# Kernel optimization log

Measured on AMD Instinct MI355X. Metric: run time of the kernel, lower is better.

## Reference

```python
import jax, jax.numpy as jnp
import numpy as np

# MPO config: input_size = output_size = 4096 = 16**3, num_cores = 3, rank = 16
D_IN = 16    # in_leg_dim
D_OUT = 16   # out_leg_dim
RANK = 16
IN_SIZE = D_IN ** 3
OUT_SIZE = D_OUT ** 3
B = 2048     # flattened batch*seq tokens


def setup_inputs() -> dict:
    key = jax.random.key(0)
    ks = jax.random.split(key, 5)
    bound = 1.0 / np.sqrt(IN_SIZE)
    u = lambda k, shp: jax.random.uniform(k, shp, jnp.float32, -bound, bound)
    return {
        "x": jax.random.normal(ks[0], (B, IN_SIZE), dtype=jnp.float32),
        "first_core": u(ks[1], (D_IN, RANK, D_OUT)),        # (in, rank_right, out)
        "middle_core": u(ks[2], (D_IN, RANK, RANK, D_OUT)),  # (in, rank_left, rank_right, out)
        "last_core": u(ks[3], (D_IN, RANK, D_OUT)),          # (in, rank_left, out)
        "bias": u(ks[4], (OUT_SIZE,)),
    }


def reference(x, first_core, middle_core, last_core, bias):
    # Faithful MPO chain contraction, same edge wiring and order as the
    # tensornetwork-based original (contract input legs left-to-right,
    # threading the bond/rank index through the cores).
    xr = x.reshape(-1, D_IN, D_IN, D_IN)                       # (b, i, j, k)
    # contract input leg i with first core -> legs (b, j, k, r, m)
    t = jnp.einsum('bijk,irm->bjkrm', xr, first_core)
    # contract input leg j and bond r with middle core -> (b, k, m, s, n)
    t = jnp.einsum('bjkrm,jrsn->bkmsn', t, middle_core)
    # contract input leg k and bond s with last core -> (b, m, n, o)
    t = jnp.einsum('bkmsn,kso->bmno', t, last_core)
    return t.reshape(-1, OUT_SIZE) + bias
```

## Files before the change

### kernel.cpp

```cpp
#include <hip/hip_runtime.h>

#define DLEG 16
#define IN_SIZE 4096
#define OUT_SIZE 4096
#define BATCH 2048

#define SX 25.4f
#define SW 1.1545455e6f

typedef __attribute__((ext_vector_type(4))) int i32x4;

__device__ __forceinline__ signed char f2i8(float f, float s) {
  int q = __float2int_rn(f * s);
  q = q > 127 ? 127 : (q < -127 ? -127 : q);
  return (signed char)q;
}

__device__ __forceinline__ void async_copy16(const void* g, void* l) {
  __builtin_amdgcn_global_load_lds(
      (const __attribute__((address_space(1))) void*)g,
      (__attribute__((address_space(3))) void*)l, 16, 0, 0);
}

__global__ __launch_bounds__(256) void k_cvt(const float* __restrict__ x,
                                             signed char* __restrict__ xi) {
  const int idx = blockIdx.x * 256 + threadIdx.x;
  const float4* xp = (const float4*)x + (size_t)idx * 4;
  union { int4 v; signed char c[16]; } u;
#pragma unroll
  for (int q = 0; q < 4; ++q) {
    const float4 f = xp[q];
    u.c[q * 4 + 0] = f2i8(f.x, SX);
    u.c[q * 4 + 1] = f2i8(f.y, SX);
    u.c[q * 4 + 2] = f2i8(f.z, SX);
    u.c[q * 4 + 3] = f2i8(f.w, SX);
  }
  ((int4*)xi)[idx] = u.v;
}

__global__ __launch_bounds__(256) void k_build_wt(
    const float* __restrict__ fc, const float* __restrict__ mc,
    const float* __restrict__ lc, signed char* __restrict__ wt) {
  __shared__ float fc_s[256];
  __shared__ float mc_s[4096];
  __shared__ float a_s[1024];
  const int b = blockIdx.x;
  const int mg = blockIdx.y;
  const int i = b >> 4, j = b & 15;
  const int t = threadIdx.x;

  fc_s[t] = fc[i * 256 + t];
#pragma unroll
  for (int q = 0; q < 16; ++q) mc_s[q * 256 + t] = mc[j * 4096 + q * 256 + t];
  __syncthreads();

  {
    const int n = t >> 4, s = t & 15;
    float accm[4] = {0.f, 0.f, 0.f, 0.f};
#pragma unroll
    for (int r = 0; r < 16; ++r) {
      const float mcv = mc_s[r * 256 + s * 16 + n];
#pragma unroll
      for (int ml = 0; ml < 4; ++ml)
        accm[ml] = fmaf(fc_s[r * 16 + mg * 4 + ml], mcv, accm[ml]);
    }
#pragma unroll
    for (int ml = 0; ml < 4; ++ml) a_s[ml * 256 + n * 16 + s] = accm[ml];
  }
  __syncthreads();

  const int k = t & 15, op = (t >> 4) & 3, sel = t >> 6;
  float lcr[4][16];
#pragma unroll
  for (int oo = 0; oo < 4; ++oo)
#pragma unroll
    for (int s = 0; s < 16; ++s)
      lcr[oo][s] = lc[k * 256 + s * 16 + op * 4 + oo];

#pragma unroll
  for (int ml = 0; ml < 4; ++ml) {
#pragma unroll
    for (int nn = 0; nn < 4; ++nn) {
      const int n = sel * 4 + nn;
      const float4* ap = (const float4*)&a_s[ml * 256 + n * 16];
      float av[16];
      ((float4*)av)[0] = ap[0];
      ((float4*)av)[1] = ap[1];
      ((float4*)av)[2] = ap[2];
      ((float4*)av)[3] = ap[3];
      float accv[4] = {0.f, 0.f, 0.f, 0.f};
#pragma unroll
      for (int s = 0; s < 16; ++s) {
#pragma unroll
        for (int oo = 0; oo < 4; ++oo)
          accv[oo] = fmaf(av[s], lcr[oo][s], accv[oo]);
      }
      const size_t colbase =
          (size_t)((mg * 4 + ml) * 256 + n * 16 + op * 4);
#pragma unroll
      for (int oo = 0; oo < 4; ++oo)
        wt[(colbase + oo) * 4096 + b * 16 + k] = f2i8(accv[oo], SW);
    }
  }
}

__global__ __launch_bounds__(256, 2) void k_gemm(
    const signed char* __restrict__ X,
    const signed char* __restrict__ Wt,
    const float* __restrict__ bias,
    float* __restrict__ out) {
  __shared__ signed char As[2][128 * 128];
  __shared__ signed char Bs[2][128 * 128];

  const int t = threadIdx.x;
  const int l = t & 63, w = t >> 6;
  const int wm = w >> 1, wn = w & 1;
  const int m0 = blockIdx.y * 128, n0 = blockIdx.x * 128;

  const signed char* xg[4];
  const signed char* wg[4];
  int ldsoff[4];
#pragma unroll
  for (int u = 0; u < 4; ++u) {
    const int c = u * 256 + t;
    const int row = c >> 3;
    const int slot = (c & 7) ^ (row & 7);
    xg[u] = X + (size_t)(m0 + row) * 4096 + slot * 16;
    wg[u] = Wt + (size_t)(n0 + row) * 4096 + slot * 16;
    ldsoff[u] = c * 16;
  }

  const int arow = wm * 64 + (l & 15);
  const int brow = wn * 64 + (l & 15);
  const int lk = l >> 4;
  const int lx = l & 7;

  i32x4 acc[4][4];
#pragma unroll
  for (int a = 0; a < 4; ++a)
#pragma unroll
    for (int c = 0; c < 4; ++c) acc[a][c] = (i32x4){0, 0, 0, 0};

#pragma unroll
  for (int u = 0; u < 4; ++u) async_copy16(xg[u], As[0] + ldsoff[u]);
#pragma unroll
  for (int u = 0; u < 4; ++u) async_copy16(wg[u], Bs[0] + ldsoff[u]);

  for (int kt = 0; kt < 4096; kt += 128) {
    const int cur = (kt >> 7) & 1;
    __syncthreads();
    if (kt + 128 < 4096) {
#pragma unroll
      for (int u = 0; u < 4; ++u)
        async_copy16(xg[u] + kt + 128, As[cur ^ 1] + ldsoff[u]);
#pragma unroll
      for (int u = 0; u < 4; ++u)
        async_copy16(wg[u] + kt + 128, Bs[cur ^ 1] + ldsoff[u]);
    }

#pragma unroll
    for (int ks = 0; ks < 2; ++ks) {
      const int slot = ((ks * 4 + lk) ^ lx) * 16;
      i32x4 af[4], bf[4];
#pragma unroll
      for (int mi = 0; mi < 4; ++mi)
        af[mi] = *(const i32x4*)&As[cur][(arow + mi * 16) * 128 + slot];
#pragma unroll
      for (int ni = 0; ni < 4; ++ni)
        bf[ni] = *(const i32x4*)&Bs[cur][(brow + ni * 16) * 128 + slot];
#pragma unroll
      for (int mi = 0; mi < 4; ++mi)
#pragma unroll
        for (int ni = 0; ni < 4; ++ni)
          acc[mi][ni] = __builtin_amdgcn_mfma_i32_16x16x64_i8(
              af[mi], bf[ni], acc[mi][ni], 0, 0, 0);
    }
  }

  const float inv = 1.0f / (SX * SW);
#pragma unroll
  for (int ni = 0; ni < 4; ++ni) {
    const int col = n0 + wn * 64 + ni * 16 + (l & 15);
    const float bv = bias[col];
#pragma unroll
    for (int mi = 0; mi < 4; ++mi) {
      const int row = m0 + wm * 64 + mi * 16 + (l >> 4) * 4;
#pragma unroll
      for (int r = 0; r < 4; ++r)
        out[(size_t)(row + r) * 4096 + col] =
            (float)acc[mi][ni][r] * inv + bv;
    }
  }
}

extern "C" void kernel_launch(void* const* d_in, const int* in_sizes, int n_in,
                              void* d_out, int out_size, void* d_ws,
                              size_t ws_size, hipStream_t stream) {
  const float* x    = (const float*)d_in[0];
  const float* fc   = (const float*)d_in[1];
  const float* mc   = (const float*)d_in[2];
  const float* lc   = (const float*)d_in[3];
  const float* bias = (const float*)d_in[4];
  float* out = (float*)d_out;

  signed char* xi = (signed char*)d_ws;
  signed char* wt = xi + (size_t)BATCH * IN_SIZE;

  k_cvt<<<(BATCH * IN_SIZE / 16) / 256, 256, 0, stream>>>(x, xi);
  k_build_wt<<<dim3(256, 4), 256, 0, stream>>>(fc, mc, lc, wt);
  k_gemm<<<dim3(OUT_SIZE / 128, BATCH / 128), 256, 0, stream>>>(xi, wt, bias, out);
}
```

Before: 152.3 us.

## Merge prep kernels into one launch and halve GEMM K-tile for occupancy

The input quantization and weight-building kernels become one launch, with block index choosing the path, which saves a launch and lets both kinds of work run at the same time. The int8 GEMM K-tile shrinks from 128 to 64, which cuts LDS use to 32KB per block, and launch bounds rise to 4 blocks per CU. The LDS swizzle changes to a 4-slot XOR to match. In exchange there are twice as many K iterations and barriers, with less work between syncs to hide load latency.

New measurement: 159.1 us. 4.4% more time.

```diff
diff --git a/kernel.cpp b/kernel.cpp
--- a/kernel.cpp
+++ b/kernel.cpp
@@ -22,32 +22,35 @@
       (__attribute__((address_space(3))) void*)l, 16, 0, 0);
 }
 
-__global__ __launch_bounds__(256) void k_cvt(const float* __restrict__ x,
-                                             signed char* __restrict__ xi) {
-  const int idx = blockIdx.x * 256 + threadIdx.x;
-  const float4* xp = (const float4*)x + (size_t)idx * 4;
-  union { int4 v; signed char c[16]; } u;
-#pragma unroll
-  for (int q = 0; q < 4; ++q) {
-    const float4 f = xp[q];
-    u.c[q * 4 + 0] = f2i8(f.x, SX);
-    u.c[q * 4 + 1] = f2i8(f.y, SX);
-    u.c[q * 4 + 2] = f2i8(f.z, SX);
-    u.c[q * 4 + 3] = f2i8(f.w, SX);
-  }
-  ((int4*)xi)[idx] = u.v;
-}
-
-__global__ __launch_bounds__(256) void k_build_wt(
-    const float* __restrict__ fc, const float* __restrict__ mc,
-    const float* __restrict__ lc, signed char* __restrict__ wt) {
+__global__ __launch_bounds__(256) void k_prep(
+    const float* __restrict__ x, const float* __restrict__ fc,
+    const float* __restrict__ mc, const float* __restrict__ lc,
+    signed char* __restrict__ xi, signed char* __restrict__ wt) {
   __shared__ float fc_s[256];
   __shared__ float mc_s[4096];
   __shared__ float a_s[1024];
-  const int b = blockIdx.x;
-  const int mg = blockIdx.y;
+  const int t = threadIdx.x;
+
+  if (blockIdx.x < 2048) {
+    const int idx = blockIdx.x * 256 + t;
+    const float4* xp = (const float4*)x + (size_t)idx * 4;
+    union { int4 v; signed char c[16]; } u;
+#pragma unroll
+    for (int q = 0; q < 4; ++q) {
+      const float4 f = xp[q];
+      u.c[q * 4 + 0] = f2i8(f.x, SX);
+      u.c[q * 4 + 1] = f2i8(f.y, SX);
+      u.c[q * 4 + 2] = f2i8(f.z, SX);
+      u.c[q * 4 + 3] = f2i8(f.w, SX);
+    }
+    ((int4*)xi)[idx] = u.v;
+    return;
+  }
+
+  const int idx = blockIdx.x - 2048;
+  const int b = idx & 255;
+  const int mg = idx >> 8;
   const int i = b >> 4, j = b & 15;
-  const int t = threadIdx.x;
 
   fc_s[t] = fc[i * 256 + t];
 #pragma unroll
@@ -104,27 +107,27 @@
   }
 }
 
-__global__ __launch_bounds__(256, 2) void k_gemm(
+__global__ __launch_bounds__(256, 4) void k_gemm(
     const signed char* __restrict__ X,
     const signed char* __restrict__ Wt,
     const float* __restrict__ bias,
     float* __restrict__ out) {
-  __shared__ signed char As[2][128 * 128];
-  __shared__ signed char Bs[2][128 * 128];
+  __shared__ signed char As[2][128 * 64];
+  __shared__ signed char Bs[2][128 * 64];
 
   const int t = threadIdx.x;
   const int l = t & 63, w = t >> 6;
   const int wm = w >> 1, wn = w & 1;
   const int m0 = blockIdx.y * 128, n0 = blockIdx.x * 128;
 
-  const signed char* xg[4];
-  const signed char* wg[4];
-  int ldsoff[4];
-#pragma unroll
-  for (int u = 0; u < 4; ++u) {
+  const signed char* xg[2];
+  const signed char* wg[2];
+  int ldsoff[2];
+#pragma unroll
+  for (int u = 0; u < 2; ++u) {
     const int c = u * 256 + t;
-    const int row = c >> 3;
-    const int slot = (c & 7) ^ (row & 7);
+    const int row = c >> 2;
+    const int slot = (c & 3) ^ (row & 3);
     xg[u] = X + (size_t)(m0 + row) * 4096 + slot * 16;
     wg[u] = Wt + (size_t)(n0 + row) * 4096 + slot * 16;
     ldsoff[u] = c * 16;
@@ -132,8 +135,7 @@
 
   const int arow = wm * 64 + (l & 15);
   const int brow = wn * 64 + (l & 15);
-  const int lk = l >> 4;
-  const int lx = l & 7;
+  const int koff = (((l >> 4) ^ (l & 3)) & 3) * 16;
 
   i32x4 acc[4][4];
 #pragma unroll
@@ -142,39 +144,35 @@
     for (int c = 0; c < 4; ++c) acc[a][c] = (i32x4){0, 0, 0, 0};
 
 #pragma unroll
-  for (int u = 0; u < 4; ++u) async_copy16(xg[u], As[0] + ldsoff[u]);
-#pragma unroll
-  for (int u = 0; u < 4; ++u) async_copy16(wg[u], Bs[0] + ldsoff[u]);
-
-  for (int kt = 0; kt < 4096; kt += 128) {
-    const int cur = (kt >> 7) & 1;
+  for (int u = 0; u < 2; ++u) async_copy16(xg[u], As[0] + ldsoff[u]);
+#pragma unroll
+  for (int u = 0; u < 2; ++u) async_copy16(wg[u], Bs[0] + ldsoff[u]);
+
+  for (int kt = 0; kt < 4096; kt += 64) {
+    const int cur = (kt >> 6) & 1;
     __syncthreads();
-    if (kt + 128 < 4096) {
-#pragma unroll
-      for (int u = 0; u < 4; ++u)
-        async_copy16(xg[u] + kt + 128, As[cur ^ 1] + ldsoff[u]);
-#pragma unroll
-      for (int u = 0; u < 4; ++u)
-        async_copy16(wg[u] + kt + 128, Bs[cur ^ 1] + ldsoff[u]);
-    }
-
-#pragma unroll
-    for (int ks = 0; ks < 2; ++ks) {
-      const int slot = ((ks * 4 + lk) ^ lx) * 16;
-      i32x4 af[4], bf[4];
-#pragma unroll
-      for (int mi = 0; mi < 4; ++mi)
-        af[mi] = *(const i32x4*)&As[cur][(arow + mi * 16) * 128 + slot];
+    if (kt + 64 < 4096) {
+#pragma unroll
+      for (int u = 0; u < 2; ++u)
+        async_copy16(xg[u] + kt + 64, As[cur ^ 1] + ldsoff[u]);
+#pragma unroll
+      for (int u = 0; u < 2; ++u)
+        async_copy16(wg[u] + kt + 64, Bs[cur ^ 1] + ldsoff[u]);
+    }
+
+    i32x4 af[4], bf[4];
+#pragma unroll
+    for (int mi = 0; mi < 4; ++mi)
+      af[mi] = *(const i32x4*)&As[cur][(arow + mi * 16) * 64 + koff];
+#pragma unroll
+    for (int ni = 0; ni < 4; ++ni)
+      bf[ni] = *(const i32x4*)&Bs[cur][(brow + ni * 16) * 64 + koff];
+#pragma unroll
+    for (int mi = 0; mi < 4; ++mi)
 #pragma unroll
       for (int ni = 0; ni < 4; ++ni)
-        bf[ni] = *(const i32x4*)&Bs[cur][(brow + ni * 16) * 128 + slot];
-#pragma unroll
-      for (int mi = 0; mi < 4; ++mi)
-#pragma unroll
-        for (int ni = 0; ni < 4; ++ni)
-          acc[mi][ni] = __builtin_amdgcn_mfma_i32_16x16x64_i8(
-              af[mi], bf[ni], acc[mi][ni], 0, 0, 0);
-    }
+        acc[mi][ni] = __builtin_amdgcn_mfma_i32_16x16x64_i8(
+            af[mi], bf[ni], acc[mi][ni], 0, 0, 0);
   }
 
   const float inv = 1.0f / (SX * SW);
@@ -206,7 +204,6 @@
   signed char* xi = (signed char*)d_ws;
   signed char* wt = xi + (size_t)BATCH * IN_SIZE;
 
-  k_cvt<<<(BATCH * IN_SIZE / 16) / 256, 256, 0, stream>>>(x, xi);
-  k_build_wt<<<dim3(256, 4), 256, 0, stream>>>(fc, mc, lc, wt);
+  k_prep<<<2048 + 1024, 256, 0, stream>>>(x, fc, mc, lc, xi, wt);
   k_gemm<<<dim3(OUT_SIZE / 128, BATCH / 128), 256, 0, stream>>>(xi, wt, bias, out);
 }
```
